# Kernel optimization log

Measured on AMD Instinct MI355X. Metric: run time of the kernel, lower is better.

Reference implementation:

```python
import jax, jax.numpy as jnp
import numpy as np

B, T_DEC, T_ENC = 64, 128, 256
D_X, N_HIDDEN, N_FEED = 1024, 1024, 1024


def _glorot(key, shape):
    fan_in = shape[0]
    return jax.random.normal(key, shape, dtype=jnp.float32) / np.sqrt(fan_in)


def setup_inputs() -> dict:
    key = jax.random.key(0)
    ks = jax.random.split(key, 10)
    H = N_HIDDEN
    return {
        "x": jax.random.normal(ks[0], (B, T_DEC, D_X), dtype=jnp.float32),
        "o_enc": jax.random.normal(ks[1], (B, T_ENC, H), dtype=jnp.float32),
        "h_enc": jax.random.normal(ks[2], (B, H), dtype=jnp.float32),
        # input-feeding FFN: Dense(n_feed, tanh), input dim = n_hidden
        "Wfeed": _glorot(ks[3], (H, N_FEED)),
        "bfeed": jnp.zeros((N_FEED,), dtype=jnp.float32),
        # GRU (keras v2, reset_after=True): kernel [n_feed+d_x, 3H], recurrent [H, 3H]
        "Wx": _glorot(ks[4], (N_FEED + D_X, 3 * H)),
        "Wh": _glorot(ks[5], (H, 3 * H)),
        "bxi": jnp.zeros((3 * H,), dtype=jnp.float32),  # input bias
        "bhr": jnp.zeros((3 * H,), dtype=jnp.float32),  # recurrent bias (reset_after)
        # attention FFN: Dense(n_hidden, tanh), input dim = 2H (concat[value, h_dec])
        "Watt": _glorot(ks[6], (2 * H, H)),
        "batt": jnp.zeros((H,), dtype=jnp.float32),
    }


def reference(x, o_enc, h_enc, Wfeed, bfeed, Wx, Wh, bxi, bhr, Watt, batt):
    # x: [B, T_dec, d_x], o_enc: [B, T_enc, H], h_enc: [B, H]
    def step(carry, x_t):
        h, i_feed = carry  # h: [B,H] GRU state, i_feed: [B,H] previous attention output
        # input feeding FFN + concat with current token
        i_cat = jnp.concatenate([jnp.tanh(i_feed @ Wfeed + bfeed), x_t], axis=-1)
        # GRU cell (keras reset_after=True semantics)
        gx = i_cat @ Wx + bxi  # [B, 3H]
        gh = h @ Wh + bhr      # [B, 3H]
        xz, xr, xh = jnp.split(gx, 3, axis=-1)
        hz, hr, hh = jnp.split(gh, 3, axis=-1)
        z = jax.nn.sigmoid(xz + hz)
        r = jax.nn.sigmoid(xr + hr)
        hcand = jnp.tanh(xh + r * hh)
        h_new = z * h + (1.0 - z) * hcand  # [B, H]
        # Luong dot attention over encoder outputs
        scores = jnp.einsum('bh,bth->bt', h_new, o_enc)       # [B, T_enc]
        attn = jax.nn.softmax(scores, axis=-1)
        value = jnp.einsum('bt,bth->bh', attn, o_enc)         # [B, H]
        h_att = jnp.tanh(jnp.concatenate([value, h_new], axis=-1) @ Watt + batt)
        return (h_new, h_att), h_att

    i_feed0 = jnp.zeros_like(h_enc)
    x_t_major = jnp.swapaxes(x, 0, 1)  # [T_dec, B, d_x]
    _, outs = jax.lax.scan(step, (h_enc, i_feed0), x_t_major)
    return jnp.swapaxes(outs, 0, 1)  # [B, T_dec, H]
```

## Files before the change

### kernel.cpp

```cpp
#include <hip/hip_runtime.h>
#include <hip/hip_bf16.h>


#define NWG 256
#define NTHR 256
constexpr int BB = 64, TD = 128, TE = 256, HH = 1024, H3 = 3072;

typedef __attribute__((ext_vector_type(8))) __bf16 bf16x8;
typedef __attribute__((ext_vector_type(4))) float f32x4;
using bf = __hip_bfloat16;

__device__ __forceinline__ f32x4 mfma16(bf16x8 a, bf16x8 b, f32x4 c) {
  return __builtin_amdgcn_mfma_f32_16x16x32_bf16(a, b, c, 0, 0, 0);
}

struct Args {
  const float *x, *o_enc, *bfeed, *bxi, *bhr, *batt;
  const bf *Wf0, *Wf1, *Wf2, *Wh0, *Wh1, *Wh2;
  const bf *WxF0, *WxF1, *WxF2, *WxX0, *WxX1, *WxX2, *Wa0, *Wa1, *Wa2;
  float *h_f32;
  float *gxp;
  float *gh, *scores;
  bf *hs0, *hs1, *hs2, *ff0, *ff1, *ff2, *ifd0, *ifd1, *ifd2;
  bf *xt0, *xt1, *xt2, *vl0, *vl1, *vl2;
  unsigned *cnt, *cnt2, *go, *afl;
  float *out;
};

__device__ __forceinline__ void gbar(unsigned ep, const Args& a, int wg) {
  __syncthreads();
  if (threadIdx.x == 0) {
    __threadfence();
    unsigned* sub = a.cnt + (wg & 15) * 32;
    unsigned o = __hip_atomic_fetch_add(sub, 1u, __ATOMIC_ACQ_REL, __HIP_MEMORY_SCOPE_AGENT);
    if (o == 15) {
      __hip_atomic_store(sub, 0u, __ATOMIC_RELAXED, __HIP_MEMORY_SCOPE_AGENT);
      unsigned o2 = __hip_atomic_fetch_add(a.cnt2, 1u, __ATOMIC_ACQ_REL, __HIP_MEMORY_SCOPE_AGENT);
      if (o2 == 15) {
        __hip_atomic_store(a.cnt2, 0u, __ATOMIC_RELAXED, __HIP_MEMORY_SCOPE_AGENT);
        __hip_atomic_store(a.go, ep, __ATOMIC_RELEASE, __HIP_MEMORY_SCOPE_AGENT);
      }
    }
    while (__hip_atomic_load(a.go, __ATOMIC_RELAXED, __HIP_MEMORY_SCOPE_AGENT) < ep)
      __builtin_amdgcn_s_sleep(2);
    __threadfence();
  }
  __syncthreads();
}

__device__ __forceinline__ void split3_write(bf* p0, bf* p1, bf* p2, size_t i, float v) {
  bf b0 = __float2bfloat16(v);
  float r1 = v - __bfloat162float(b0);
  bf b1 = __float2bfloat16(r1);
  float r2 = r1 - __bfloat162float(b1);
  p0[i] = b0; p1[i] = b1; p2[i] = __float2bfloat16(r2);
}

template <int K>
__device__ __forceinline__ f32x4 gemm6(const bf* A0, const bf* A1, const bf* A2,
                                       const bf* B0, const bf* B1, const bf* B2) {
  f32x4 c0 = {0.f, 0.f, 0.f, 0.f}, c1 = c0, c2 = c0, c3 = c0;
#pragma unroll 4
  for (int k = 0; k < K; k += 32) {
    bf16x8 a0 = *(const bf16x8*)(A0 + k);
    bf16x8 a1 = *(const bf16x8*)(A1 + k);
    bf16x8 a2 = *(const bf16x8*)(A2 + k);
    bf16x8 b0 = *(const bf16x8*)(B0 + k);
    bf16x8 b1 = *(const bf16x8*)(B1 + k);
    bf16x8 b2 = *(const bf16x8*)(B2 + k);
    c0 = mfma16(a0, b0, c0);
    c1 = mfma16(a0, b1, c1);
    c2 = mfma16(a1, b0, c2);
    c3 = mfma16(a1, b1, c3);
    c0 = mfma16(a0, b2, c0);
    c1 = mfma16(a2, b0, c1);
  }
  f32x4 s;
#pragma unroll
  for (int i = 0; i < 4; ++i) s[i] = (c0[i] + c1[i]) + (c2[i] + c3[i]);
  return s;
}

__global__ __launch_bounds__(NTHR, 1) void decoder_main(Args a) {
  const int wg = blockIdx.x;
  const int tid = threadIdx.x;
  const int lane = tid & 63;
  const int wv = tid >> 6;
  const int lrow = lane & 15;
  const int lkg = lane >> 4;

  __shared__ float s_h[HH];
  __shared__ float s_part[64][4];
  __shared__ float s_sm[TE];
  __shared__ float s_red[8];

  unsigned ep = 0;

  for (int t = 0; t < TD; ++t) {
    {
      const bool isf = (wg < 64);
      const int j0 = (isf ? wg : wg - 64) * 16;
      const bf* A0 = isf ? a.ifd0 : a.hs0;
      const bf* A1 = isf ? a.ifd1 : a.hs1;
      const bf* A2 = isf ? a.ifd2 : a.hs2;
      const bf* B0 = isf ? a.Wf0 : a.Wh0;
      const bf* B1 = isf ? a.Wf1 : a.Wh1;
      const bf* B2 = isf ? a.Wf2 : a.Wh2;
      const size_t aoff = (size_t)(16 * wv + lrow) * HH + lkg * 8;
      const size_t boff = (size_t)(j0 + lrow) * HH + lkg * 8;
      f32x4 acc = gemm6<HH>(A0 + aoff, A1 + aoff, A2 + aoff, B0 + boff, B1 + boff, B2 + boff);
      const int col = j0 + lrow;
      if (isf) {
        float bia = a.bfeed[col];
#pragma unroll
        for (int r = 0; r < 4; ++r) {
          int row2 = 16 * wv + lkg * 4 + r;
          float f = tanhf(acc[r] + bia);
          split3_write(a.ff0, a.ff1, a.ff2, (size_t)row2 * HH + col, f);
        }
      } else {
        float bia = a.bhr[col];
#pragma unroll
        for (int r = 0; r < 4; ++r) {
          int row2 = 16 * wv + lkg * 4 + r;
          a.gh[(size_t)row2 * H3 + col] = acc[r] + bia;
        }
      }
    }
    gbar(++ep, a, wg);

    {
      const int jt = wg >> 2, kq = wg & 3;
      const int j0 = jt * 16;
      const bool isff = (kq < 2);
      const int koff = (kq & 1) * 512;
      const bf* A0 = isff ? a.ff0 : a.xt0;
      const bf* A1 = isff ? a.ff1 : a.xt1;
      const bf* A2 = isff ? a.ff2 : a.xt2;
      const bf* B0 = isff ? a.WxF0 : a.WxX0;
      const bf* B1 = isff ? a.WxF1 : a.WxX1;
      const bf* B2 = isff ? a.WxF2 : a.WxX2;
#pragma unroll
      for (int u = wv * 3; u < wv * 3 + 3; ++u) {
        const int g = u >> 2, mt = u & 3;
        const size_t aoff = (size_t)(mt * 16 + lrow) * HH + koff + lkg * 8;
        const size_t boff = (size_t)(g * HH + j0 + lrow) * HH + koff + lkg * 8;
        f32x4 acc = gemm6<512>(A0 + aoff, A1 + aoff, A2 + aoff, B0 + boff, B1 + boff, B2 + boff);
        const int gcol = g * HH + j0 + lrow;
#pragma unroll
        for (int r = 0; r < 4; ++r) {
          int grow = mt * 16 + lkg * 4 + r;
          a.gxp[(size_t)(kq * 64 + grow) * H3 + gcol] = acc[r];
        }
      }
    }
    gbar(++ep, a, wg);

    {
      const int b = wg >> 2, q = wg & 3;
      const float* hold = a.h_f32 + (size_t)(t & 1) * (BB * HH);
      float* hnew = a.h_f32 + (size_t)((t + 1) & 1) * (BB * HH);
      const float* ghb = a.gh + (size_t)b * H3;
#pragma unroll
      for (int i = 0; i < 4; ++i) {
        const int col = i * 256 + tid;
        float gz = a.bxi[col], gr = a.bxi[HH + col], gc = a.bxi[2 * HH + col];
#pragma unroll
        for (int kq = 0; kq < 4; ++kq) {
          const float* gp = a.gxp + (size_t)(kq * 64 + b) * H3;
          gz += gp[col]; gr += gp[HH + col]; gc += gp[2 * HH + col];
        }
        float z = 1.f / (1.f + expf(-(gz + ghb[col])));
        float rr = 1.f / (1.f + expf(-(gr + ghb[HH + col])));
        float hc = tanhf(gc + rr * ghb[2 * HH + col]);
        float hn = z * hold[(size_t)b * HH + col] + (1.f - z) * hc;
        s_h[col] = hn;
        if (q == 0) {
          hnew[(size_t)b * HH + col] = hn;
          split3_write(a.hs0, a.hs1, a.hs2, (size_t)b * HH + col, hn);
        }
      }
      __syncthreads();
      {
        const int tt = tid & 63, kq4 = tid >> 6;
        const int tg = q * 64 + tt;
        const float* orow = a.o_enc + ((size_t)b * TE + tg) * HH + kq4 * 256;
        const float* hp = s_h + kq4 * 256;
        float s = 0.f;
        for (int k = 0; k < 256; k += 4) {
          f32x4 o4 = *(const f32x4*)(orow + k);
          s += o4[0] * hp[k] + o4[1] * hp[k + 1] + o4[2] * hp[k + 2] + o4[3] * hp[k + 3];
        }
        s_part[tt][kq4] = s;
      }
      __syncthreads();
      if (tid < 64)
        a.scores[(size_t)b * TE + q * 64 + tid] =
            s_part[tid][0] + s_part[tid][1] + s_part[tid][2] + s_part[tid][3];
      __syncthreads();
      if (tid == 0) {
        __threadfence();
        __hip_atomic_store(&a.afl[b * 4 + q], (unsigned)(t + 1),
                           __ATOMIC_RELEASE, __HIP_MEMORY_SCOPE_AGENT);
        for (int p = 1; p < 4; ++p) {
          unsigned idx = b * 4 + ((q + p) & 3);
          while (__hip_atomic_load(&a.afl[idx], __ATOMIC_RELAXED, __HIP_MEMORY_SCOPE_AGENT)
                 < (unsigned)(t + 1))
            __builtin_amdgcn_s_sleep(1);
        }
        __threadfence();
      }
      __syncthreads();
      float sc = a.scores[(size_t)b * TE + tid];
      float v = sc;
      for (int off = 32; off; off >>= 1) v = fmaxf(v, __shfl_xor(v, off));
      if (lane == 0) s_red[wv] = v;
      __syncthreads();
      float mx = fmaxf(fmaxf(s_red[0], s_red[1]), fmaxf(s_red[2], s_red[3]));
      float p = expf(sc - mx);
      float sum = p;
      for (int off = 32; off; off >>= 1) sum += __shfl_xor(sum, off);
      if (lane == 0) s_red[4 + wv] = sum;
      __syncthreads();
      float tot = s_red[4] + s_red[5] + s_red[6] + s_red[7];
      s_sm[tid] = p / tot;
      __syncthreads();
      {
        const int j = q * 256 + tid;
        const float* ob = a.o_enc + (size_t)b * TE * HH + j;
        float accv = 0.f;
        for (int tt2 = 0; tt2 < TE; ++tt2) {
          float w2 = s_sm[tt2];
          if (w2 > 1e-8f) accv += w2 * ob[(size_t)tt2 * HH];
        }
        split3_write(a.vl0, a.vl1, a.vl2, (size_t)b * HH + j, accv);
      }
    }
    gbar(++ep, a, wg);

    {
      const int cu = wg >> 2, kq = wg & 3;
      const int j0 = cu * 16;
      const bool isv = (kq < 2);
      const int koff = (kq & 1) * 512;
      const bf* A0 = isv ? a.vl0 : a.hs0;
      const bf* A1 = isv ? a.vl1 : a.hs1;
      const bf* A2 = isv ? a.vl2 : a.hs2;
      const size_t aoff = (size_t)(16 * wv + lrow) * HH + koff + lkg * 8;
      const size_t boff = (size_t)(j0 + lrow) * 2048 + kq * 512 + lkg * 8;
      f32x4 acc = gemm6<512>(A0 + aoff, A1 + aoff, A2 + aoff,
                             a.Wa0 + boff, a.Wa1 + boff, a.Wa2 + boff);
      const int col = j0 + lrow;
#pragma unroll
      for (int r = 0; r < 4; ++r) {
        int row2 = 16 * wv + lkg * 4 + r;
        a.gxp[(size_t)(kq * 64 + row2) * 1024 + col] = acc[r];
      }
    }
    gbar(++ep, a, wg);

    {
      const int id = wg * NTHR + tid;
      const int row = id >> 10, col = id & 1023;
      float s = a.batt[col];
#pragma unroll
      for (int kq = 0; kq < 4; ++kq) s += a.gxp[(size_t)(kq * 64 + row) * 1024 + col];
      float hv = tanhf(s);
      a.out[((size_t)row * TD + t) * HH + col] = hv;
      split3_write(a.ifd0, a.ifd1, a.ifd2, (size_t)row * HH + col, hv);
      if (t + 1 < TD) {
        float xv = a.x[((size_t)row * TD + (t + 1)) * HH + col];
        split3_write(a.xt0, a.xt1, a.xt2, (size_t)id, xv);
      }
    }
    gbar(++ep, a, wg);
  }
}

__global__ void k_tr3(const float* src, bf* d0, bf* d1, bf* d2, int R, int C) {
  __shared__ float tile[32][33];
  int c0 = blockIdx.x * 32, r0 = blockIdx.y * 32;
  int tx = threadIdx.x & 31, ty = threadIdx.x >> 5;
  for (int i = ty; i < 32; i += 8)
    tile[i][tx] = src[(size_t)(r0 + i) * C + c0 + tx];
  __syncthreads();
  for (int i = ty; i < 32; i += 8) {
    float v = tile[tx][i];
    size_t o = (size_t)(c0 + i) * R + r0 + tx;
    bf b0 = __float2bfloat16(v);
    float r1 = v - __bfloat162float(b0);
    bf b1 = __float2bfloat16(r1);
    d0[o] = b0; d1[o] = b1; d2[o] = __float2bfloat16(r1 - __bfloat162float(b1));
  }
}

__global__ void k_init(const float* h_enc, float* h_f32, bf* h0, bf* h1, bf* h2,
                       bf* i0, bf* i1, bf* i2, const float* x, bf* x0, bf* x1, bf* x2) {
  int i = blockIdx.x * blockDim.x + threadIdx.x;
  float v = h_enc[i];
  h_f32[i] = v;
  split3_write(h0, h1, h2, i, v);
  bf z = __float2bfloat16(0.f);
  i0[i] = z; i1[i] = z; i2[i] = z;
  int row = i >> 10, col = i & 1023;
  split3_write(x0, x1, x2, i, x[((size_t)row * TD + 0) * HH + col]);
}

extern "C" void kernel_launch(void* const* d_in, const int* in_sizes, int n_in,
                              void* d_out, int out_size, void* d_ws, size_t ws_size,
                              hipStream_t stream) {
  const float* x     = (const float*)d_in[0];
  const float* o_enc = (const float*)d_in[1];
  const float* h_enc = (const float*)d_in[2];
  const float* Wfeed = (const float*)d_in[3];
  const float* bfeed = (const float*)d_in[4];
  const float* Wx    = (const float*)d_in[5];
  const float* Wh    = (const float*)d_in[6];
  const float* bxi   = (const float*)d_in[7];
  const float* bhr   = (const float*)d_in[8];
  const float* Watt  = (const float*)d_in[9];
  const float* batt  = (const float*)d_in[10];

  char* w = (char*)d_ws;
  auto alloc = [&](size_t b) { char* p = w; w += (b + 255) & ~255ULL; return p; };

  const size_t M1 = (size_t)1024 * 1024 * 2;
  bf* Wf[3];  for (auto& p : Wf)  p = (bf*)alloc(M1);
  bf* Wh_[3]; for (auto& p : Wh_) p = (bf*)alloc(3 * M1);
  bf* WxF[3]; for (auto& p : WxF) p = (bf*)alloc(3 * M1);
  bf* WxX[3]; for (auto& p : WxX) p = (bf*)alloc(3 * M1);
  bf* Wa[3];  for (auto& p : Wa)  p = (bf*)alloc(2 * M1);
  float* h_f32  = (float*)alloc((size_t)2 * BB * HH * 4);
  float* gxp    = (float*)alloc((size_t)4 * BB * H3 * 4);
  float* gh     = (float*)alloc((size_t)BB * H3 * 4);
  float* scores = (float*)alloc((size_t)BB * TE * 4);
  const size_t AB = (size_t)BB * HH * 2;
  bf *hs[3], *ff[3], *ifd[3], *xt[3], *vl[3];
  for (auto& p : hs)  p = (bf*)alloc(AB);
  for (auto& p : ff)  p = (bf*)alloc(AB);
  for (auto& p : ifd) p = (bf*)alloc(AB);
  for (auto& p : xt)  p = (bf*)alloc(AB);
  for (auto& p : vl)  p = (bf*)alloc(AB);
  unsigned* flags = (unsigned*)alloc(8192);

  hipMemsetAsync(flags, 0, 8192, stream);
  k_tr3<<<dim3(32, 32), 256, 0, stream>>>(Wfeed, Wf[0], Wf[1], Wf[2], 1024, 1024);
  k_tr3<<<dim3(96, 32), 256, 0, stream>>>(Wx, WxF[0], WxF[1], WxF[2], 1024, 3072);
  k_tr3<<<dim3(96, 32), 256, 0, stream>>>(Wx + (size_t)1024 * 3072, WxX[0], WxX[1], WxX[2], 1024, 3072);
  k_tr3<<<dim3(96, 32), 256, 0, stream>>>(Wh, Wh_[0], Wh_[1], Wh_[2], 1024, 3072);
  k_tr3<<<dim3(32, 64), 256, 0, stream>>>(Watt, Wa[0], Wa[1], Wa[2], 2048, 1024);
  k_init<<<BB * HH / 256, 256, 0, stream>>>(h_enc, h_f32, hs[0], hs[1], hs[2],
                                            ifd[0], ifd[1], ifd[2], x, xt[0], xt[1], xt[2]);

  Args a;
  a.x = x; a.o_enc = o_enc; a.bfeed = bfeed; a.bxi = bxi; a.bhr = bhr; a.batt = batt;
  a.Wf0 = Wf[0]; a.Wf1 = Wf[1]; a.Wf2 = Wf[2];
  a.Wh0 = Wh_[0]; a.Wh1 = Wh_[1]; a.Wh2 = Wh_[2];
  a.WxF0 = WxF[0]; a.WxF1 = WxF[1]; a.WxF2 = WxF[2];
  a.WxX0 = WxX[0]; a.WxX1 = WxX[1]; a.WxX2 = WxX[2];
  a.Wa0 = Wa[0]; a.Wa1 = Wa[1]; a.Wa2 = Wa[2];
  a.h_f32 = h_f32; a.gxp = gxp; a.gh = gh; a.scores = scores;
  a.hs0 = hs[0]; a.hs1 = hs[1]; a.hs2 = hs[2];
  a.ff0 = ff[0]; a.ff1 = ff[1]; a.ff2 = ff[2];
  a.ifd0 = ifd[0]; a.ifd1 = ifd[1]; a.ifd2 = ifd[2];
  a.xt0 = xt[0]; a.xt1 = xt[1]; a.xt2 = xt[2];
  a.vl0 = vl[0]; a.vl1 = vl[1]; a.vl2 = vl[2];
  a.cnt = flags; a.cnt2 = flags + 512; a.go = flags + 544; a.afl = flags + 576;
  a.out = (float*)d_out;

  decoder_main<<<NWG, NTHR, 0, stream>>>(a);
}
```

Before: 25.66 ms.

## Double workgroup size and repartition every persistent-kernel phase across eight waves

```diff
diff --git a/kernel.cpp b/kernel.cpp
--- a/kernel.cpp
+++ b/kernel.cpp
@@ -3,7 +3,7 @@
 
 
 #define NWG 256
-#define NTHR 256
+#define NTHR 512
 constexpr int BB = 64, TD = 128, TE = 256, HH = 1024, H3 = 3072;
 
 typedef __attribute__((ext_vector_type(8))) __bf16 bf16x8;
@@ -81,7 +81,7 @@
   return s;
 }
 
-__global__ __launch_bounds__(NTHR, 1) void decoder_main(Args a) {
+__global__ __launch_bounds__(NTHR, 2) void decoder_main(Args a) {
   const int wg = blockIdx.x;
   const int tid = threadIdx.x;
   const int lane = tid & 63;
@@ -89,10 +89,11 @@
   const int lrow = lane & 15;
   const int lkg = lane >> 4;
 
+  __shared__ float s_acc[2][4][16][16];
   __shared__ float s_h[HH];
-  __shared__ float s_part[64][4];
   __shared__ float s_sm[TE];
   __shared__ float s_red[8];
+  __shared__ float s_val[2][256];
 
   unsigned ep = 0;
 
@@ -106,53 +107,48 @@
       const bf* B0 = isf ? a.Wf0 : a.Wh0;
       const bf* B1 = isf ? a.Wf1 : a.Wh1;
       const bf* B2 = isf ? a.Wf2 : a.Wh2;
-      const size_t aoff = (size_t)(16 * wv + lrow) * HH + lkg * 8;
-      const size_t boff = (size_t)(j0 + lrow) * HH + lkg * 8;
-      f32x4 acc = gemm6<HH>(A0 + aoff, A1 + aoff, A2 + aoff, B0 + boff, B1 + boff, B2 + boff);
-      const int col = j0 + lrow;
-      if (isf) {
-        float bia = a.bfeed[col];
-#pragma unroll
-        for (int r = 0; r < 4; ++r) {
-          int row2 = 16 * wv + lkg * 4 + r;
-          float f = tanhf(acc[r] + bia);
-          split3_write(a.ff0, a.ff1, a.ff2, (size_t)row2 * HH + col, f);
-        }
-      } else {
-        float bia = a.bhr[col];
-#pragma unroll
-        for (int r = 0; r < 4; ++r) {
-          int row2 = 16 * wv + lkg * 4 + r;
-          a.gh[(size_t)row2 * H3 + col] = acc[r] + bia;
-        }
-      }
-    }
-    gbar(++ep, a, wg);
-
-    {
-      const int jt = wg >> 2, kq = wg & 3;
-      const int j0 = jt * 16;
-      const bool isff = (kq < 2);
-      const int koff = (kq & 1) * 512;
-      const bf* A0 = isff ? a.ff0 : a.xt0;
-      const bf* A1 = isff ? a.ff1 : a.xt1;
-      const bf* A2 = isff ? a.ff2 : a.xt2;
-      const bf* B0 = isff ? a.WxF0 : a.WxX0;
-      const bf* B1 = isff ? a.WxF1 : a.WxX1;
-      const bf* B2 = isff ? a.WxF2 : a.WxX2;
-#pragma unroll
-      for (int u = wv * 3; u < wv * 3 + 3; ++u) {
-        const int g = u >> 2, mt = u & 3;
-        const size_t aoff = (size_t)(mt * 16 + lrow) * HH + koff + lkg * 8;
-        const size_t boff = (size_t)(g * HH + j0 + lrow) * HH + koff + lkg * 8;
-        f32x4 acc = gemm6<512>(A0 + aoff, A1 + aoff, A2 + aoff, B0 + boff, B1 + boff, B2 + boff);
-        const int gcol = g * HH + j0 + lrow;
-#pragma unroll
-        for (int r = 0; r < 4; ++r) {
-          int grow = mt * 16 + lkg * 4 + r;
-          a.gxp[(size_t)(kq * 64 + grow) * H3 + gcol] = acc[r];
-        }
-      }
+      const int mt = wv & 3, kh = wv >> 2;
+      const size_t aoff = (size_t)(mt * 16 + lrow) * HH + kh * 512 + lkg * 8;
+      const size_t boff = (size_t)(j0 + lrow) * HH + kh * 512 + lkg * 8;
+      f32x4 acc = gemm6<512>(A0 + aoff, A1 + aoff, A2 + aoff, B0 + boff, B1 + boff, B2 + boff);
+#pragma unroll
+      for (int r = 0; r < 4; ++r) s_acc[kh][mt][lkg * 4 + r][lrow] = acc[r];
+      __syncthreads();
+#pragma unroll
+      for (int e = tid; e < 1024; e += NTHR) {
+        const int row = e >> 4, c = e & 15;
+        const int emt = row >> 4, err2 = row & 15;
+        float v = s_acc[0][emt][err2][c] + s_acc[1][emt][err2][c];
+        const int col = j0 + c;
+        if (isf) {
+          float f = tanhf(v + a.bfeed[col]);
+          split3_write(a.ff0, a.ff1, a.ff2, (size_t)row * HH + col, f);
+        } else {
+          a.gh[(size_t)row * H3 + col] = v + a.bhr[col];
+        }
+      }
+    }
+    gbar(++ep, a, wg);
+
+    if (wv < 6) {
+      const int unit = wg * 6 + wv;
+      const int kh2 = unit & 1;
+      const int jt = (unit >> 1) & 63;
+      const int gm = unit >> 7;
+      const int g = gm >> 2, mt = gm & 3;
+      const bf* A0 = kh2 ? a.xt0 : a.ff0;
+      const bf* A1 = kh2 ? a.xt1 : a.ff1;
+      const bf* A2 = kh2 ? a.xt2 : a.ff2;
+      const bf* B0 = kh2 ? a.WxX0 : a.WxF0;
+      const bf* B1 = kh2 ? a.WxX1 : a.WxF1;
+      const bf* B2 = kh2 ? a.WxX2 : a.WxF2;
+      const size_t aoff = (size_t)(mt * 16 + lrow) * HH + lkg * 8;
+      const size_t boff = (size_t)(g * HH + jt * 16 + lrow) * HH + lkg * 8;
+      f32x4 acc = gemm6<1024>(A0 + aoff, A1 + aoff, A2 + aoff, B0 + boff, B1 + boff, B2 + boff);
+      const int gcol = g * 1024 + jt * 16 + lrow;
+#pragma unroll
+      for (int r = 0; r < 4; ++r)
+        a.gxp[(size_t)(kh2 * 64 + mt * 16 + lkg * 4 + r) * H3 + gcol] = acc[r];
     }
     gbar(++ep, a, wg);
 
@@ -162,14 +158,13 @@
       float* hnew = a.h_f32 + (size_t)((t + 1) & 1) * (BB * HH);
       const float* ghb = a.gh + (size_t)b * H3;
 #pragma unroll
-      for (int i = 0; i < 4; ++i) {
-        const int col = i * 256 + tid;
-        float gz = a.bxi[col], gr = a.bxi[HH + col], gc = a.bxi[2 * HH + col];
-#pragma unroll
-        for (int kq = 0; kq < 4; ++kq) {
-          const float* gp = a.gxp + (size_t)(kq * 64 + b) * H3;
-          gz += gp[col]; gr += gp[HH + col]; gc += gp[2 * HH + col];
-        }
+      for (int ii = 0; ii < 2; ++ii) {
+        const int col = ii * NTHR + tid;
+        const float* g0 = a.gxp + (size_t)b * H3;
+        const float* g1 = a.gxp + (size_t)(64 + b) * H3;
+        float gz = a.bxi[col] + g0[col] + g1[col];
+        float gr = a.bxi[HH + col] + g0[HH + col] + g1[HH + col];
+        float gc = a.bxi[2 * HH + col] + g0[2 * HH + col] + g1[2 * HH + col];
         float z = 1.f / (1.f + expf(-(gz + ghb[col])));
         float rr = 1.f / (1.f + expf(-(gr + ghb[HH + col])));
         float hc = tanhf(gc + rr * ghb[2 * HH + col]);
@@ -182,21 +177,26 @@
       }
       __syncthreads();
       {
-        const int tt = tid & 63, kq4 = tid >> 6;
-        const int tg = q * 64 + tt;
-        const float* orow = a.o_enc + ((size_t)b * TE + tg) * HH + kq4 * 256;
-        const float* hp = s_h + kq4 * 256;
-        float s = 0.f;
-        for (int k = 0; k < 256; k += 4) {
-          f32x4 o4 = *(const f32x4*)(orow + k);
-          s += o4[0] * hp[k] + o4[1] * hp[k + 1] + o4[2] * hp[k + 2] + o4[3] * hp[k + 3];
-        }
-        s_part[tt][kq4] = s;
-      }
-      __syncthreads();
-      if (tid < 64)
-        a.scores[(size_t)b * TE + q * 64 + tid] =
-            s_part[tid][0] + s_part[tid][1] + s_part[tid][2] + s_part[tid][3];
+        f32x4 sh0 = *(const f32x4*)(s_h + 0 + lane * 4);
+        f32x4 sh1 = *(const f32x4*)(s_h + 256 + lane * 4);
+        f32x4 sh2 = *(const f32x4*)(s_h + 512 + lane * 4);
+        f32x4 sh3 = *(const f32x4*)(s_h + 768 + lane * 4);
+        const float* obase = a.o_enc + ((size_t)b * TE + q * 64 + wv * 8) * HH + lane * 4;
+#pragma unroll 2
+        for (int i = 0; i < 8; ++i) {
+          const float* orow = obase + (size_t)i * HH;
+          f32x4 o0 = *(const f32x4*)(orow);
+          f32x4 o1 = *(const f32x4*)(orow + 256);
+          f32x4 o2 = *(const f32x4*)(orow + 512);
+          f32x4 o3 = *(const f32x4*)(orow + 768);
+          float s = o0[0] * sh0[0] + o0[1] * sh0[1] + o0[2] * sh0[2] + o0[3] * sh0[3]
+                  + o1[0] * sh1[0] + o1[1] * sh1[1] + o1[2] * sh1[2] + o1[3] * sh1[3]
+                  + o2[0] * sh2[0] + o2[1] * sh2[1] + o2[2] * sh2[2] + o2[3] * sh2[3]
+                  + o3[0] * sh3[0] + o3[1] * sh3[1] + o3[2] * sh3[2] + o3[3] * sh3[3];
+          for (int off = 32; off; off >>= 1) s += __shfl_xor(s, off);
+          if (lane == 0) a.scores[(size_t)b * TE + q * 64 + wv * 8 + i] = s;
+        }
+      }
       __syncthreads();
       if (tid == 0) {
         __threadfence();
@@ -211,66 +211,81 @@
         __threadfence();
       }
       __syncthreads();
-      float sc = a.scores[(size_t)b * TE + tid];
-      float v = sc;
-      for (int off = 32; off; off >>= 1) v = fmaxf(v, __shfl_xor(v, off));
-      if (lane == 0) s_red[wv] = v;
-      __syncthreads();
-      float mx = fmaxf(fmaxf(s_red[0], s_red[1]), fmaxf(s_red[2], s_red[3]));
-      float p = expf(sc - mx);
-      float sum = p;
-      for (int off = 32; off; off >>= 1) sum += __shfl_xor(sum, off);
-      if (lane == 0) s_red[4 + wv] = sum;
-      __syncthreads();
-      float tot = s_red[4] + s_red[5] + s_red[6] + s_red[7];
-      s_sm[tid] = p / tot;
+      float sc = 0.f, p = 0.f;
+      if (tid < 256) {
+        sc = a.scores[(size_t)b * TE + tid];
+        float v = sc;
+        for (int off = 32; off; off >>= 1) v = fmaxf(v, __shfl_xor(v, off));
+        if (lane == 0) s_red[wv] = v;
+      }
       __syncthreads();
       {
-        const int j = q * 256 + tid;
+        float mx = fmaxf(fmaxf(s_red[0], s_red[1]), fmaxf(s_red[2], s_red[3]));
+        if (tid < 256) {
+          p = expf(sc - mx);
+          float sum = p;
+          for (int off = 32; off; off >>= 1) sum += __shfl_xor(sum, off);
+          if (lane == 0) s_red[4 + wv] = sum;
+        }
+      }
+      __syncthreads();
+      if (tid < 256) {
+        float tot = s_red[4] + s_red[5] + s_red[6] + s_red[7];
+        s_sm[tid] = p / tot;
+      }
+      __syncthreads();
+      {
+        const int c = tid & 255, th = tid >> 8;
+        const int j = q * 256 + c;
         const float* ob = a.o_enc + (size_t)b * TE * HH + j;
         float accv = 0.f;
-        for (int tt2 = 0; tt2 < TE; ++tt2) {
+        for (int tt2 = th * 128; tt2 < th * 128 + 128; ++tt2) {
           float w2 = s_sm[tt2];
           if (w2 > 1e-8f) accv += w2 * ob[(size_t)tt2 * HH];
         }
-        split3_write(a.vl0, a.vl1, a.vl2, (size_t)b * HH + j, accv);
-      }
+        s_val[th][c] = accv;
+      }
+      __syncthreads();
+      if (tid < 256)
+        split3_write(a.vl0, a.vl1, a.vl2, (size_t)b * HH + q * 256 + tid,
+                     s_val[0][tid] + s_val[1][tid]);
     }
     gbar(++ep, a, wg);
 
     {
-      const int cu = wg >> 2, kq = wg & 3;
-      const int j0 = cu * 16;
-      const bool isv = (kq < 2);
-      const int koff = (kq & 1) * 512;
+      const int kq8 = wv;
+      const int cu = wg & 63;
+      const int mt = wg >> 6;
+      const bool isv = (kq8 < 4);
+      const int koff = (kq8 & 3) * 256;
       const bf* A0 = isv ? a.vl0 : a.hs0;
       const bf* A1 = isv ? a.vl1 : a.hs1;
       const bf* A2 = isv ? a.vl2 : a.hs2;
-      const size_t aoff = (size_t)(16 * wv + lrow) * HH + koff + lkg * 8;
-      const size_t boff = (size_t)(j0 + lrow) * 2048 + kq * 512 + lkg * 8;
-      f32x4 acc = gemm6<512>(A0 + aoff, A1 + aoff, A2 + aoff,
+      const size_t aoff = (size_t)(mt * 16 + lrow) * HH + koff + lkg * 8;
+      const size_t boff = (size_t)(cu * 16 + lrow) * 2048 + kq8 * 256 + lkg * 8;
+      f32x4 acc = gemm6<256>(A0 + aoff, A1 + aoff, A2 + aoff,
                              a.Wa0 + boff, a.Wa1 + boff, a.Wa2 + boff);
-      const int col = j0 + lrow;
-#pragma unroll
-      for (int r = 0; r < 4; ++r) {
-        int row2 = 16 * wv + lkg * 4 + r;
-        a.gxp[(size_t)(kq * 64 + row2) * 1024 + col] = acc[r];
-      }
+#pragma unroll
+      for (int r = 0; r < 4; ++r)
+        a.gxp[(size_t)(kq8 * 64 + mt * 16 + lkg * 4 + r) * 1024 + cu * 16 + lrow] = acc[r];
     }
     gbar(++ep, a, wg);
 
     {
       const int id = wg * NTHR + tid;
-      const int row = id >> 10, col = id & 1023;
-      float s = a.batt[col];
-#pragma unroll
-      for (int kq = 0; kq < 4; ++kq) s += a.gxp[(size_t)(kq * 64 + row) * 1024 + col];
-      float hv = tanhf(s);
-      a.out[((size_t)row * TD + t) * HH + col] = hv;
-      split3_write(a.ifd0, a.ifd1, a.ifd2, (size_t)row * HH + col, hv);
-      if (t + 1 < TD) {
-        float xv = a.x[((size_t)row * TD + (t + 1)) * HH + col];
-        split3_write(a.xt0, a.xt1, a.xt2, (size_t)id, xv);
+      if (id < 65536) {
+        const int row = id >> 10, col = id & 1023;
+        float s = a.batt[col];
+#pragma unroll
+        for (int kq = 0; kq < 8; ++kq) s += a.gxp[(size_t)(kq * 64 + row) * 1024 + col];
+        float hv = tanhf(s);
+        a.out[((size_t)row * TD + t) * HH + col] = hv;
+        split3_write(a.ifd0, a.ifd1, a.ifd2, (size_t)row * HH + col, hv);
+      } else if (t + 1 < TD) {
+        const int id2 = id - 65536;
+        const int row = id2 >> 10, col = id2 & 1023;
+        split3_write(a.xt0, a.xt1, a.xt2, (size_t)id2,
+                     a.x[((size_t)row * TD + (t + 1)) * HH + col]);
       }
     }
     gbar(++ep, a, wg);
@@ -331,7 +346,7 @@
   bf* WxX[3]; for (auto& p : WxX) p = (bf*)alloc(3 * M1);
   bf* Wa[3];  for (auto& p : Wa)  p = (bf*)alloc(2 * M1);
   float* h_f32  = (float*)alloc((size_t)2 * BB * HH * 4);
-  float* gxp    = (float*)alloc((size_t)4 * BB * H3 * 4);
+  float* gxp    = (float*)alloc((size_t)8 * BB * H3 * 4);
   float* gh     = (float*)alloc((size_t)BB * H3 * 4);
   float* scores = (float*)alloc((size_t)BB * TE * 4);
   const size_t AB = (size_t)BB * HH * 2;
```

After: 24.12 ms. 6.0% less time.
